# Performance work log

Hardware: AMD Instinct MI355X
Metric: run time of the kernel (lower is better)

## Reference

```python
import jax, jax.numpy as jnp
import numpy as np

HEADS = 8
DIM_HEAD = 64
INNER = HEADS * DIM_HEAD  # 512
EPS = 1e-6


def layer_norm(x, gamma, beta):
    mu = jnp.mean(x, axis=-1, keepdims=True)
    var = jnp.var(x, axis=-1, keepdims=True)
    return (x - mu) * jax.lax.rsqrt(var + EPS) * gamma + beta


def setup_inputs() -> dict:
    key = jax.random.key(0)
    ks = jax.random.split(key, 8)
    b, n = 2, 2048
    s = lambda d: 1.0 / np.sqrt(d)
    return {
        "x": jax.random.normal(ks[0], (b, n, INNER), dtype=jnp.float32),
        # weights stored input-major: y = x @ W
        "w_qkv": jax.random.normal(ks[1], (INNER, 3 * INNER), dtype=jnp.float32) * s(INNER),
        "w_out": jax.random.normal(ks[2], (INNER, INNER), dtype=jnp.float32) * s(INNER),
        "b_out": jax.random.normal(ks[3], (INNER,), dtype=jnp.float32) * 0.01,
        "w_ff1": jax.random.normal(ks[4], (INNER, 4 * INNER), dtype=jnp.float32) * s(INNER),
        "w_ff2": jax.random.normal(ks[5], (4 * INNER, INNER), dtype=jnp.float32) * s(4 * INNER),
        "g1": jnp.ones((INNER,), dtype=jnp.float32),
        "be1": jnp.zeros((INNER,), dtype=jnp.float32),
        "g2": jnp.ones((INNER,), dtype=jnp.float32),
        "be2": jnp.zeros((INNER,), dtype=jnp.float32),
    }


def reference(x, w_qkv, w_out, b_out, w_ff1, w_ff2, g1, be1, g2, be2):
    b, n, _ = x.shape
    scale = DIM_HEAD ** (-0.5)
    qkv = x @ w_qkv  # [b, n, 3*inner]
    qkv = qkv.reshape(b, n, 3, HEADS, DIM_HEAD)
    q = qkv[:, :, 0].transpose(0, 2, 1, 3)  # [b, h, n, d]
    k = qkv[:, :, 1].transpose(0, 2, 1, 3)
    v = qkv[:, :, 2].transpose(0, 2, 1, 3)
    dots = jnp.einsum('bhqd,bhkd->bhqk', q, k) * scale
    attn = jax.nn.softmax(dots, axis=-1)
    out = jnp.einsum('bhqk,bhkd->bhqd', attn, v)
    out = out.transpose(0, 2, 1, 3).reshape(b, n, INNER)
    out = out @ w_out + b_out
    attn_res = layer_norm(x + out, g1, be1)
    # NOTE: no activation between the two FFN linears (faithful to source)
    ff = (attn_res @ w_ff1) @ w_ff2
    return layer_norm(attn_res + ff, g2, be2)
```

## Files before the change

### kernel.cpp

```cpp
#include <hip/hip_runtime.h>
#include <hip/hip_bf16.h>
#include <cstdint>
#include <cstddef>
#include <math.h>

#define HEADS 8
#define DHEAD 64
#define INNER 512
#define BATCH 2
#define SEQ   2048
#define MROWS (BATCH*SEQ)
#define LN_EPS 1e-6f
#define KSPLIT 4
#define KCHUNK (SEQ/KSPLIT)
#define QSCALE 0.18033688011110918f

typedef unsigned short u16;
typedef __attribute__((ext_vector_type(8))) short short8;
typedef __attribute__((ext_vector_type(4))) short short4v;
typedef __attribute__((ext_vector_type(4))) float f32x4;

#define MFMA16(a,b,c) __builtin_amdgcn_mfma_f32_16x16x32_bf16((a),(b),(c),0,0,0)
#if __has_builtin(__builtin_amdgcn_mfma_f32_16x16x16bf16_1k)
#define HAVE_MFMA16K16 1
#define MFMA16K16(a,b,c) __builtin_amdgcn_mfma_f32_16x16x16bf16_1k((a),(b),(c),0,0,0)
#endif

__device__ __forceinline__ float bf2f(u16 u) {
    union { float f; uint32_t i; } x; x.i = ((uint32_t)u) << 16; return x.f;
}
__device__ __forceinline__ u16 f2bf(float f) {
    __hip_bfloat16 h = __float2bfloat16(f);
    return *reinterpret_cast<u16*>(&h);
}
__device__ __forceinline__ void gl_lds16(const void* g, void* l) {
    __builtin_amdgcn_global_load_lds(
        (const __attribute__((address_space(1))) void*)g,
        (__attribute__((address_space(3))) void*)l, 16, 0, 0);
}

__global__ void prep_kernel(const float* __restrict__ x, u16* __restrict__ x_b,
                            const float* __restrict__ w_qkv, u16* __restrict__ w_qkvT,
                            const float* __restrict__ w_out, u16* __restrict__ w_outT,
                            const float* __restrict__ w_ff1, u16* __restrict__ w_ff1T,
                            const float* __restrict__ w_ff2, u16* __restrict__ w_ff2T) {
    __shared__ float T[32][33];
    const int blk = blockIdx.x, tid = threadIdx.x;
    if (blk < 2048) {
        int i = blk * 256 + tid;
        float4 v = reinterpret_cast<const float4*>(x)[i];
        ushort4 o;
        o.x = f2bf(v.x); o.y = f2bf(v.y); o.z = f2bf(v.z); o.w = f2bf(v.w);
        reinterpret_cast<ushort4*>(x_b)[i] = o;
        return;
    }
    const float* B; u16* Bt; int K, N, t;
    if (blk < 2816)      { B = w_qkv; Bt = w_qkvT; K = 512;  N = 1536; t = blk - 2048; }
    else if (blk < 3072) { B = w_out; Bt = w_outT; K = 512;  N = 512;  t = blk - 2816; }
    else if (blk < 4096) { B = w_ff1; Bt = w_ff1T; K = 512;  N = 2048; t = blk - 3072; }
    else                 { B = w_ff2; Bt = w_ff2T; K = 2048; N = 512;  t = blk - 4096; }
    const int nb = N / 32;
    const int n0 = (t % nb) * 32, k0 = (t / nb) * 32;
    const int r = tid >> 3, c = (tid & 7) * 4;
    float4 v = *reinterpret_cast<const float4*>(&B[(size_t)(k0 + r) * N + n0 + c]);
    T[c + 0][r] = v.x; T[c + 1][r] = v.y; T[c + 2][r] = v.z; T[c + 3][r] = v.w;
    __syncthreads();
    ushort4 o;
    o.x = f2bf(T[r][c + 0]); o.y = f2bf(T[r][c + 1]);
    o.z = f2bf(T[r][c + 2]); o.w = f2bf(T[r][c + 3]);
    *reinterpret_cast<ushort4*>(&Bt[(size_t)(n0 + r) * K + k0 + c]) = o;
}

template<int BN, int BK, int EPI>
__global__ __launch_bounds__(256) void gemm_bt(const u16* __restrict__ A,
                                               const u16* __restrict__ Bt,
                                               u16* __restrict__ Cb,
                                               u16* __restrict__ Vt,
                                               int M, int N, int K) {
    constexpr int WN = BN / 2;
    constexpr int NT = WN / 16;
    constexpr int ACH = 128 * BK / 8;
    constexpr int BCH = BN * BK / 8;
    constexpr int CW = BK / 8;
    __shared__ u16 As[128 * BK];
    __shared__ u16 Bs[BN * BK];
    const int tid = threadIdx.x;
    const int wave = tid >> 6, lane = tid & 63;
    const int l15 = lane & 15, quad = lane >> 4;
    const int wm = (wave >> 1) * 64, wn = (wave & 1) * WN;
    const int row0 = blockIdx.y * 128, col0 = blockIdx.x * BN;

    int kbase = 0, kend = K;
    if (EPI == 3) {
        int chunk = K / gridDim.z;
        kbase = blockIdx.z * chunk; kend = kbase + chunk;
    }

    f32x4 acc[4][NT];
    #pragma unroll
    for (int mi = 0; mi < 4; ++mi)
        #pragma unroll
        for (int ni = 0; ni < NT; ++ni)
            #pragma unroll
            for (int e = 0; e < 4; ++e) acc[mi][ni][e] = 0.f;

    for (int k0 = kbase; k0 < kend; k0 += BK) {
        #pragma unroll
        for (int idx0 = 0; idx0 < ACH + BCH; idx0 += 256) {
            int idx = idx0 + tid;
            if (idx < ACH) {
                int r = idx / CW, ic = (idx % CW) * 8;
                gl_lds16(A + (size_t)(row0 + r) * K + k0 + ic, &As[idx * 8]);
            } else {
                int ib = idx - ACH;
                int r = ib / CW, ic = (ib % CW) * 8;
                gl_lds16(Bt + (size_t)(col0 + r) * K + k0 + ic, &Bs[ib * 8]);
            }
        }
        __syncthreads();

        #pragma unroll
        for (int ks2 = 0; ks2 < BK / 32; ++ks2) {
            short8 af[4], bfr[NT];
            #pragma unroll
            for (int mi = 0; mi < 4; ++mi)
                af[mi] = *reinterpret_cast<const short8*>(
                    &As[(wm + mi * 16 + l15) * BK + ks2 * 32 + quad * 8]);
            #pragma unroll
            for (int ni = 0; ni < NT; ++ni)
                bfr[ni] = *reinterpret_cast<const short8*>(
                    &Bs[(wn + ni * 16 + l15) * BK + ks2 * 32 + quad * 8]);
            #pragma unroll
            for (int mi = 0; mi < 4; ++mi)
                #pragma unroll
                for (int ni = 0; ni < NT; ++ni)
                    acc[mi][ni] = MFMA16(af[mi], bfr[ni], acc[mi][ni]);
        }
        __syncthreads();
    }

    #pragma unroll
    for (int mi = 0; mi < 4; ++mi)
        #pragma unroll
        for (int ni = 0; ni < NT; ++ni) {
            const int cc = col0 + wn + ni * 16 + l15;
            const int rr0 = row0 + wm + mi * 16 + quad * 4;
            if (EPI == 0) {
                #pragma unroll
                for (int r = 0; r < 4; ++r)
                    Cb[(size_t)(rr0 + r) * N + cc] = f2bf(acc[mi][ni][r]);
            } else if (EPI == 3) {
                u16* Cz = Cb + (size_t)blockIdx.z * M * N;
                #pragma unroll
                for (int r = 0; r < 4; ++r)
                    Cz[(size_t)(rr0 + r) * N + cc] = f2bf(acc[mi][ni][r]);
            } else {
                if (cc < 1024) {
                    const bool isq = (cc < 512);
                    size_t base = isq ? (size_t)cc
                                      : ((size_t)MROWS * 512 + cc - 512);
                    const float sc = isq ? QSCALE : 1.f;
                    #pragma unroll
                    for (int r = 0; r < 4; ++r)
                        Cb[base + (size_t)(rr0 + r) * 512] = f2bf(acc[mi][ni][r] * sc);
                } else {
                    int hh = (cc - 1024) >> 6, dd = (cc - 1024) & 63;
                    int bb = rr0 >> 11, srow = rr0 & 2047;
                    ushort4 o;
                    o.x = f2bf(acc[mi][ni][0]); o.y = f2bf(acc[mi][ni][1]);
                    o.z = f2bf(acc[mi][ni][2]); o.w = f2bf(acc[mi][ni][3]);
                    *reinterpret_cast<ushort4*>(
                        &Vt[(((size_t)(bb * 8 + hh) * 64 + dd) << 11) + srow]) = o;
                }
            }
        }
}

__global__ __launch_bounds__(256) void attn_kernel(const u16* __restrict__ qk_b,
                                                   const u16* __restrict__ vT_b,
                                                   u16* __restrict__ OpartB,
                                                   float* __restrict__ lpart) {
#ifdef HAVE_MFMA16K16
    __shared__ u16 SM[2 * 64 * 72];
    u16 (*Ks)[72] = (u16(*)[72])SM;
    u16 (*VT)[72] = (u16(*)[72])(SM + 64 * 72);
#else
    __shared__ u16 SM[128 * 64 + 2 * 64 * 72];
    u16 (*Qs)[64] = (u16(*)[64])SM;
    u16 (*Ks)[72] = (u16(*)[72])(SM + 128 * 64);
    u16 (*VT)[72] = (u16(*)[72])(SM + 128 * 64 + 64 * 72);
#endif

    const int tid = threadIdx.x;
    const int wave = tid >> 6, lane = tid & 63;
    const int l15 = lane & 15, quad = lane >> 4;
    const int qt = blockIdx.x, bh = blockIdx.y, ks = blockIdx.z;
    const int b = bh >> 3, h = bh & 7;
    const int w16 = wave * 16;
    const int r0 = tid >> 3, r1 = r0 + 32;
    const int ch = (tid & 7) * 8;

    const u16* qb = qk_b + (size_t)(b * SEQ + qt * 128) * 512 + h * 64;
    const u16* kb = qk_b + (size_t)MROWS * 512
                  + (size_t)(b * SEQ + ks * KCHUNK) * 512 + h * 64;
    const u16* vb = vT_b + (size_t)bh * 64 * 2048 + ks * KCHUNK;

    uint4 kr0 = *reinterpret_cast<const uint4*>(&kb[(size_t)r0 * 512 + ch]);
    uint4 kr1 = *reinterpret_cast<const uint4*>(&kb[(size_t)r1 * 512 + ch]);
    uint4 vr0 = *reinterpret_cast<const uint4*>(&vb[(size_t)r0 * 2048 + ch]);
    uint4 vr1 = *reinterpret_cast<const uint4*>(&vb[(size_t)r1 * 2048 + ch]);

#ifdef HAVE_MFMA16K16
    short8 qf[2][2];
    #pragma unroll
    for (int t = 0; t < 2; ++t)
        #pragma unroll
        for (int ksk = 0; ksk < 2; ++ksk)
            qf[t][ksk] = *reinterpret_cast<const short8*>(
                &qb[(size_t)(t * 64 + w16 + l15) * 512 + ksk * 32 + quad * 8]);

    const short ONEB = (short)0x3F80;
    const short4v ones = {ONEB, ONEB, ONEB, ONEB};

    f32x4 oacc[2][4], lacc[2];
    #pragma unroll
    for (int t = 0; t < 2; ++t) {
        #pragma unroll
        for (int di = 0; di < 4; ++di)
            #pragma unroll
            for (int e = 0; e < 4; ++e) oacc[t][di][e] = 0.f;
        #pragma unroll
        for (int e = 0; e < 4; ++e) lacc[t][e] = 0.f;
    }

    for (int kt = 0; kt < KCHUNK / 64; ++kt) {
        *reinterpret_cast<uint4*>(&Ks[r0][ch]) = kr0;
        *reinterpret_cast<uint4*>(&Ks[r1][ch]) = kr1;
        *reinterpret_cast<uint4*>(&VT[r0][ch]) = vr0;
        *reinterpret_cast<uint4*>(&VT[r1][ch]) = vr1;
        __syncthreads();

        if (kt + 1 < KCHUNK / 64) {
            const u16* kb2 = kb + (size_t)(kt + 1) * 64 * 512;
            const u16* vb2 = vb + (kt + 1) * 64;
            kr0 = *reinterpret_cast<const uint4*>(&kb2[(size_t)r0 * 512 + ch]);
            kr1 = *reinterpret_cast<const uint4*>(&kb2[(size_t)r1 * 512 + ch]);
            vr0 = *reinterpret_cast<const uint4*>(&vb2[(size_t)r0 * 2048 + ch]);
            vr1 = *reinterpret_cast<const uint4*>(&vb2[(size_t)r1 * 2048 + ch]);
        }

        short8 kf[4], kf2[4];
        #pragma unroll
        for (int ni = 0; ni < 4; ++ni) {
            kf[ni]  = *reinterpret_cast<const short8*>(&Ks[ni * 16 + l15][quad * 8]);
            kf2[ni] = *reinterpret_cast<const short8*>(&Ks[ni * 16 + l15][32 + quad * 8]);
        }

        #pragma unroll
        for (int t = 0; t < 2; ++t) {
            f32x4 sacc[4];
            #pragma unroll
            for (int ni = 0; ni < 4; ++ni)
                #pragma unroll
                for (int e = 0; e < 4; ++e) sacc[ni][e] = 0.f;
            #pragma unroll
            for (int ni = 0; ni < 4; ++ni)
                sacc[ni] = MFMA16(kf[ni], qf[t][0], sacc[ni]);
            #pragma unroll
            for (int ni = 0; ni < 4; ++ni)
                sacc[ni] = MFMA16(kf2[ni], qf[t][1], sacc[ni]);

            #pragma unroll
            for (int ni = 0; ni < 4; ++ni) {
                float p0 = exp2f(sacc[ni][0]);
                float p1 = exp2f(sacc[ni][1]);
                float p2 = exp2f(sacc[ni][2]);
                float p3 = exp2f(sacc[ni][3]);
                union { short4v v; uint32_t u[2]; } P;
                P.u[0] = __builtin_amdgcn_perm(__float_as_uint(p1),
                                               __float_as_uint(p0), 0x07060302u);
                P.u[1] = __builtin_amdgcn_perm(__float_as_uint(p3),
                                               __float_as_uint(p2), 0x07060302u);
                lacc[t] = MFMA16K16(ones, P.v, lacc[t]);
                #pragma unroll
                for (int di = 0; di < 4; ++di) {
                    short4v vf = *reinterpret_cast<const short4v*>(
                        &VT[di * 16 + l15][ni * 16 + quad * 4]);
                    oacc[t][di] = MFMA16K16(vf, P.v, oacc[t][di]);
                }
            }
        }
        __syncthreads();
    }

    const size_t pbase = ((size_t)(ks * 16 + bh) * SEQ + qt * 128);
    if (lane < 16) {
        lpart[pbase + w16 + lane]      = lacc[0][0];
        lpart[pbase + 64 + w16 + lane] = lacc[1][0];
    }

    float* OTf = (float*)SM;
    const int ql = tid >> 2, dseg = (tid & 3) * 16;
    #pragma unroll
    for (int t = 0; t < 2; ++t) {
        __syncthreads();
        #pragma unroll
        for (int di = 0; di < 4; ++di)
            #pragma unroll
            for (int r = 0; r < 4; ++r)
                OTf[(di * 16 + quad * 4 + r) * 68 + w16 + l15] = oacc[t][di][r];
        __syncthreads();
        u16 ov[16];
        #pragma unroll
        for (int i = 0; i < 16; ++i) ov[i] = f2bf(OTf[(dseg + i) * 68 + ql]);
        u16* op = &OpartB[(pbase + t * 64 + ql) * 64 + dseg];
        *reinterpret_cast<uint4*>(op)     = *reinterpret_cast<const uint4*>(ov);
        *reinterpret_cast<uint4*>(op + 8) = *reinterpret_cast<const uint4*>(ov + 8);
    }
#else
    {
        #pragma unroll
        for (int j = 0; j < 4; ++j) {
            int idx = tid + j * 256;
            int r = idx >> 3, c = (idx & 7) * 8;
            *reinterpret_cast<uint4*>(&Qs[r][c]) =
                *reinterpret_cast<const uint4*>(&qb[(size_t)r * 512 + c]);
        }
    }
    __syncthreads();

    short8 qf[2][2];
    #pragma unroll
    for (int t = 0; t < 2; ++t) {
        qf[t][0] = *reinterpret_cast<const short8*>(&Qs[t * 64 + w16 + l15][quad * 8]);
        qf[t][1] = *reinterpret_cast<const short8*>(&Qs[t * 64 + w16 + l15][32 + quad * 8]);
    }

    f32x4 oacc[2][4];
    float lsum[2][4];
    #pragma unroll
    for (int t = 0; t < 2; ++t)
        #pragma unroll
        for (int di = 0; di < 4; ++di) {
            #pragma unroll
            for (int e = 0; e < 4; ++e) oacc[t][di][e] = 0.f;
            lsum[t][di] = 0.f;
        }

    for (int kt = 0; kt < KCHUNK / 64; ++kt) {
        *reinterpret_cast<uint4*>(&Ks[r0][ch]) = kr0;
        *reinterpret_cast<uint4*>(&Ks[r1][ch]) = kr1;
        *reinterpret_cast<uint4*>(&VT[r0][ch]) = vr0;
        *reinterpret_cast<uint4*>(&VT[r1][ch]) = vr1;
        __syncthreads();

        if (kt + 1 < KCHUNK / 64) {
            const u16* kb2 = kb + (size_t)(kt + 1) * 64 * 512;
            const u16* vb2 = vb + (kt + 1) * 64;
            kr0 = *reinterpret_cast<const uint4*>(&kb2[(size_t)r0 * 512 + ch]);
            kr1 = *reinterpret_cast<const uint4*>(&kb2[(size_t)r1 * 512 + ch]);
            vr0 = *reinterpret_cast<const uint4*>(&vb2[(size_t)r0 * 2048 + ch]);
            vr1 = *reinterpret_cast<const uint4*>(&vb2[(size_t)r1 * 2048 + ch]);
        }

        #pragma unroll
        for (int t = 0; t < 2; ++t) {
            f32x4 sacc[4];
            #pragma unroll
            for (int ni = 0; ni < 4; ++ni)
                #pragma unroll
                for (int e = 0; e < 4; ++e) sacc[ni][e] = 0.f;
            #pragma unroll
            for (int ksk = 0; ksk < 2; ++ksk) {
                short8 kf[4];
                #pragma unroll
                for (int ni = 0; ni < 4; ++ni)
                    kf[ni] = *reinterpret_cast<const short8*>(
                        &Ks[ni * 16 + l15][ksk * 32 + quad * 8]);
                #pragma unroll
                for (int ni = 0; ni < 4; ++ni)
                    sacc[ni] = MFMA16(qf[t][ksk], kf[ni], sacc[ni]);
            }
            #pragma unroll
            for (int ni = 0; ni < 4; ++ni)
                #pragma unroll
                for (int r = 0; r < 4; ++r) {
                    float p = exp2f(sacc[ni][r]);
                    lsum[t][r] += p;
                    Qs[t * 64 + w16 + quad * 4 + r][ni * 16 + l15] = f2bf(p);
                }
            #pragma unroll
            for (int ksk = 0; ksk < 2; ++ksk) {
                short8 pf = *reinterpret_cast<const short8*>(
                    &Qs[t * 64 + w16 + l15][ksk * 32 + quad * 8]);
                #pragma unroll
                for (int di = 0; di < 4; ++di) {
                    short8 vf = *reinterpret_cast<const short8*>(
                        &VT[di * 16 + l15][ksk * 32 + quad * 8]);
                    oacc[t][di] = MFMA16(pf, vf, oacc[t][di]);
                }
            }
        }
        __syncthreads();
    }

    const size_t pbase = ((size_t)(ks * 16 + bh) * SEQ + qt * 128);
    #pragma unroll
    for (int t = 0; t < 2; ++t) {
        #pragma unroll
        for (int r = 0; r < 4; ++r) {
            float v = lsum[t][r];
            v += __shfl_xor(v, 1); v += __shfl_xor(v, 2);
            v += __shfl_xor(v, 4); v += __shfl_xor(v, 8);
            lsum[t][r] = v;
        }
        #pragma unroll
        for (int di = 0; di < 4; ++di)
            #pragma unroll
            for (int r = 0; r < 4; ++r)
                OpartB[(pbase + t * 64 + w16 + quad * 4 + r) * 64 + di * 16 + l15]
                    = f2bf(oacc[t][di][r]);
        if (l15 == 0)
            #pragma unroll
            for (int r = 0; r < 4; ++r)
                lpart[pbase + t * 64 + w16 + quad * 4 + r] = lsum[t][r];
    }
#endif
}

__global__ void attn_combine_kernel(const u16* __restrict__ OpartB,
                                    const float* __restrict__ lpart,
                                    u16* __restrict__ attn_b) {
    int i = blockIdx.x * 256 + threadIdx.x;
    int e = i * 4;
    int row = e >> 9;
    int c = e & 511;
    int h = c >> 6, d = c & 63;
    int b = row >> 11, srow = row & 2047;
    int bh = b * 8 + h;

    float ax = 0.f, ay = 0.f, az = 0.f, aw = 0.f, l = 0.f;
    #pragma unroll
    for (int ks = 0; ks < KSPLIT; ++ks) {
        size_t pk = (size_t)(ks * 16 + bh) * SEQ + srow;
        ushort4 o = *reinterpret_cast<const ushort4*>(&OpartB[pk * 64 + d]);
        ax += bf2f(o.x); ay += bf2f(o.y); az += bf2f(o.z); aw += bf2f(o.w);
        l += lpart[pk];
    }
    float li = 1.f / l;
    ushort4 o;
    o.x = f2bf(ax * li); o.y = f2bf(ay * li);
    o.z = f2bf(az * li); o.w = f2bf(aw * li);
    *reinterpret_cast<ushort4*>(&attn_b[(size_t)row * INNER + c]) = o;
}

template<bool A16, int NS>
__global__ __launch_bounds__(256) void ln_kernel(const void* __restrict__ a_,
                                                 const u16* __restrict__ s_,
                                                 size_t sstride,
                                                 const float* __restrict__ bias,
                                                 const float* __restrict__ g,
                                                 const float* __restrict__ be,
                                                 float* __restrict__ out32,
                                                 u16* __restrict__ out16) {
    const int tid = threadIdx.x, wave = tid >> 6, lane = tid & 63;
    const int row = blockIdx.x * 4 + wave;
    const size_t off = (size_t)row * INNER;

    float v[8];
    #pragma unroll
    for (int j = 0; j < 2; ++j) {
        const int c = j * 256 + lane * 4;
        if (A16) {
            ushort4 u = *reinterpret_cast<const ushort4*>((const u16*)a_ + off + c);
            v[j*4+0] = bf2f(u.x); v[j*4+1] = bf2f(u.y);
            v[j*4+2] = bf2f(u.z); v[j*4+3] = bf2f(u.w);
        } else {
            float4 u = *reinterpret_cast<const float4*>((const float*)a_ + off + c);
            v[j*4+0] = u.x; v[j*4+1] = u.y; v[j*4+2] = u.z; v[j*4+3] = u.w;
        }
        #pragma unroll
        for (int s = 0; s < NS; ++s) {
            ushort4 u = *reinterpret_cast<const ushort4*>(
                s_ + (size_t)s * sstride + off + c);
            v[j*4+0] += bf2f(u.x); v[j*4+1] += bf2f(u.y);
            v[j*4+2] += bf2f(u.z); v[j*4+3] += bf2f(u.w);
        }
        if (bias) {
            float4 u = *reinterpret_cast<const float4*>(bias + c);
            v[j*4+0] += u.x; v[j*4+1] += u.y; v[j*4+2] += u.z; v[j*4+3] += u.w;
        }
    }

    float s = 0.f;
    #pragma unroll
    for (int i = 0; i < 8; ++i) s += v[i];
    #pragma unroll
    for (int m = 1; m < 64; m <<= 1) s += __shfl_xor(s, m);
    const float mu = s * (1.f / INNER);

    float q = 0.f;
    #pragma unroll
    for (int i = 0; i < 8; ++i) { v[i] -= mu; q += v[i] * v[i]; }
    #pragma unroll
    for (int m = 1; m < 64; m <<= 1) q += __shfl_xor(q, m);
    const float rstd = rsqrtf(q * (1.f / INNER) + LN_EPS);

    #pragma unroll
    for (int j = 0; j < 2; ++j) {
        const int c = j * 256 + lane * 4;
        float4 gv = *reinterpret_cast<const float4*>(g + c);
        float4 bv = *reinterpret_cast<const float4*>(be + c);
        float y0 = v[j*4+0] * rstd * gv.x + bv.x;
        float y1 = v[j*4+1] * rstd * gv.y + bv.y;
        float y2 = v[j*4+2] * rstd * gv.z + bv.z;
        float y3 = v[j*4+3] * rstd * gv.w + bv.w;
        if (out32) {
            float4 o = {y0, y1, y2, y3};
            *reinterpret_cast<float4*>(out32 + off + c) = o;
        }
        if (out16) {
            ushort4 o;
            o.x = f2bf(y0); o.y = f2bf(y1); o.z = f2bf(y2); o.w = f2bf(y3);
            *reinterpret_cast<ushort4*>(out16 + off + c) = o;
        }
    }
}

extern "C" void kernel_launch(void* const* d_in, const int* in_sizes, int n_in,
                              void* d_out, int out_size, void* d_ws, size_t ws_size,
                              hipStream_t stream) {
    const float* x     = (const float*)d_in[0];
    const float* w_qkv = (const float*)d_in[1];
    const float* w_out = (const float*)d_in[2];
    const float* b_out = (const float*)d_in[3];
    const float* w_ff1 = (const float*)d_in[4];
    const float* w_ff2 = (const float*)d_in[5];
    const float* g1    = (const float*)d_in[6];
    const float* be1   = (const float*)d_in[7];
    const float* g2    = (const float*)d_in[8];
    const float* be2   = (const float*)d_in[9];
    float* out = (float*)d_out;

    char* W = (char*)d_ws;
    u16*   w_outT     = (u16*)  (W + 0);
    u16*   w_ff1T     = (u16*)  (W + 524288);
    u16*   w_ff2T     = (u16*)  (W + 2621440);
    u16*   qk_b       = (u16*)  (W + 4718592);
    u16*   projp      = (u16*)  (W + 4718592);
    u16*   vT_b       = (u16*)  (W + 13107200);
    u16*   attn_res_b = (u16*)  (W + 13107200);
    u16*   x_b        = (u16*)  (W + 17301504);
    u16*   w_qkvT     = (u16*)  (W + 21495808);
    u16*   OpartB     = (u16*)  (W + 23068672);
    float* lpart      = (float*)(W + 39845888);
    u16*   attn_b     = (u16*)  (W + 40370176);
    u16*   ff1_b      = (u16*)  (W + 17301504);
    u16*   ff2p       = (u16*)  (W + 40370176);

    prep_kernel<<<5120, 256, 0, stream>>>(x, x_b, w_qkv, w_qkvT, w_out, w_outT,
                                          w_ff1, w_ff1T, w_ff2, w_ff2T);

    gemm_bt<64, 64, 2><<<dim3(1536 / 64, MROWS / 128), 256, 0, stream>>>(
        x_b, w_qkvT, qk_b, vT_b, MROWS, 1536, INNER);

    attn_kernel<<<dim3(SEQ / 128, BATCH * HEADS, KSPLIT), 256, 0, stream>>>(
        qk_b, vT_b, OpartB, lpart);

    attn_combine_kernel<<<(MROWS * INNER / 4) / 256, 256, 0, stream>>>(
        OpartB, lpart, attn_b);

    gemm_bt<64, 64, 3><<<dim3(INNER / 64, MROWS / 128, 2), 256, 0, stream>>>(
        attn_b, w_outT, projp, nullptr, MROWS, INNER, INNER);

    ln_kernel<true, 2><<<MROWS / 4, 256, 0, stream>>>(
        x_b, projp, (size_t)MROWS * INNER, b_out, g1, be1, nullptr, attn_res_b);

    gemm_bt<128, 64, 0><<<dim3(2048 / 128, MROWS / 128), 256, 0, stream>>>(
        attn_res_b, w_ff1T, ff1_b, nullptr, MROWS, 2048, INNER);

    gemm_bt<64, 64, 3><<<dim3(INNER / 64, MROWS / 128, 4), 256, 0, stream>>>(
        ff1_b, w_ff2T, ff2p, nullptr, MROWS, INNER, 2048);

    ln_kernel<true, 4><<<MROWS / 4, 256, 0, stream>>>(
        attn_res_b, ff2p, (size_t)MROWS * INNER, nullptr, g2, be2, out, nullptr);
}
```

Measured before the change: 204.8 us.

## Shrink attention query tile to 64 and double key split to 8

The attention kernel now processes 64 query rows per block instead of 128, and the key sequence is split into 8 chunks instead of 4. The grid grows from 1024 to 4096 blocks, with less work and fewer live registers per block, to raise occupancy and parallelism. In exchange each K/V tile is loaded and reused for half as many queries, and the combine step must read and merge twice as many partial outputs. Workspace buffers are re-laid out so the larger partial-output and normalizer arrays fit.

```diff
diff --git a/kernel.cpp b/kernel.cpp
--- a/kernel.cpp
+++ b/kernel.cpp
@@ -11,7 +11,7 @@
 #define SEQ   2048
 #define MROWS (BATCH*SEQ)
 #define LN_EPS 1e-6f
-#define KSPLIT 4
+#define KSPLIT 8
 #define KCHUNK (SEQ/KSPLIT)
 #define QSCALE 0.18033688011110918f
 
@@ -185,10 +185,10 @@
     u16 (*Ks)[72] = (u16(*)[72])SM;
     u16 (*VT)[72] = (u16(*)[72])(SM + 64 * 72);
 #else
-    __shared__ u16 SM[128 * 64 + 2 * 64 * 72];
+    __shared__ u16 SM[64 * 64 + 2 * 64 * 72];
     u16 (*Qs)[64] = (u16(*)[64])SM;
-    u16 (*Ks)[72] = (u16(*)[72])(SM + 128 * 64);
-    u16 (*VT)[72] = (u16(*)[72])(SM + 128 * 64 + 64 * 72);
+    u16 (*Ks)[72] = (u16(*)[72])(SM + 64 * 64);
+    u16 (*VT)[72] = (u16(*)[72])(SM + 64 * 64 + 64 * 72);
 #endif
 
     const int tid = threadIdx.x;
@@ -199,8 +199,9 @@
     const int w16 = wave * 16;
     const int r0 = tid >> 3, r1 = r0 + 32;
     const int ch = (tid & 7) * 8;
-
-    const u16* qb = qk_b + (size_t)(b * SEQ + qt * 128) * 512 + h * 64;
+    constexpr int NT = KCHUNK / 64;
+
+    const u16* qb = qk_b + (size_t)(b * SEQ + qt * 64) * 512 + h * 64;
     const u16* kb = qk_b + (size_t)MROWS * 512
                   + (size_t)(b * SEQ + ks * KCHUNK) * 512 + h * 64;
     const u16* vb = vT_b + (size_t)bh * 64 * 2048 + ks * KCHUNK;
@@ -211,36 +212,29 @@
     uint4 vr1 = *reinterpret_cast<const uint4*>(&vb[(size_t)r1 * 2048 + ch]);
 
 #ifdef HAVE_MFMA16K16
-    short8 qf[2][2];
-    #pragma unroll
-    for (int t = 0; t < 2; ++t)
-        #pragma unroll
-        for (int ksk = 0; ksk < 2; ++ksk)
-            qf[t][ksk] = *reinterpret_cast<const short8*>(
-                &qb[(size_t)(t * 64 + w16 + l15) * 512 + ksk * 32 + quad * 8]);
+    short8 qf[2];
+    qf[0] = *reinterpret_cast<const short8*>(&qb[(size_t)(w16 + l15) * 512 + quad * 8]);
+    qf[1] = *reinterpret_cast<const short8*>(&qb[(size_t)(w16 + l15) * 512 + 32 + quad * 8]);
 
     const short ONEB = (short)0x3F80;
     const short4v ones = {ONEB, ONEB, ONEB, ONEB};
 
-    f32x4 oacc[2][4], lacc[2];
-    #pragma unroll
-    for (int t = 0; t < 2; ++t) {
-        #pragma unroll
-        for (int di = 0; di < 4; ++di)
-            #pragma unroll
-            for (int e = 0; e < 4; ++e) oacc[t][di][e] = 0.f;
-        #pragma unroll
-        for (int e = 0; e < 4; ++e) lacc[t][e] = 0.f;
-    }
-
-    for (int kt = 0; kt < KCHUNK / 64; ++kt) {
+    f32x4 oacc[4], lacc;
+    #pragma unroll
+    for (int di = 0; di < 4; ++di)
+        #pragma unroll
+        for (int e = 0; e < 4; ++e) oacc[di][e] = 0.f;
+    #pragma unroll
+    for (int e = 0; e < 4; ++e) lacc[e] = 0.f;
+
+    for (int kt = 0; kt < NT; ++kt) {
         *reinterpret_cast<uint4*>(&Ks[r0][ch]) = kr0;
         *reinterpret_cast<uint4*>(&Ks[r1][ch]) = kr1;
         *reinterpret_cast<uint4*>(&VT[r0][ch]) = vr0;
         *reinterpret_cast<uint4*>(&VT[r1][ch]) = vr1;
         __syncthreads();
 
-        if (kt + 1 < KCHUNK / 64) {
+        if (kt + 1 < NT) {
             const u16* kb2 = kb + (size_t)(kt + 1) * 64 * 512;
             const u16* vb2 = vb + (kt + 1) * 64;
             kr0 = *reinterpret_cast<const uint4*>(&kb2[(size_t)r0 * 512 + ch]);
@@ -249,78 +243,70 @@
             vr1 = *reinterpret_cast<const uint4*>(&vb2[(size_t)r1 * 2048 + ch]);
         }
 
-        short8 kf[4], kf2[4];
+        f32x4 sacc[4];
+        #pragma unroll
+        for (int ni = 0; ni < 4; ++ni)
+            #pragma unroll
+            for (int e = 0; e < 4; ++e) sacc[ni][e] = 0.f;
+        {
+            short8 kf[4], kf2[4];
+            #pragma unroll
+            for (int ni = 0; ni < 4; ++ni) {
+                kf[ni]  = *reinterpret_cast<const short8*>(&Ks[ni * 16 + l15][quad * 8]);
+                kf2[ni] = *reinterpret_cast<const short8*>(&Ks[ni * 16 + l15][32 + quad * 8]);
+            }
+            #pragma unroll
+            for (int ni = 0; ni < 4; ++ni)
+                sacc[ni] = MFMA16(kf[ni], qf[0], sacc[ni]);
+            #pragma unroll
+            for (int ni = 0; ni < 4; ++ni)
+                sacc[ni] = MFMA16(kf2[ni], qf[1], sacc[ni]);
+        }
+
         #pragma unroll
         for (int ni = 0; ni < 4; ++ni) {
-            kf[ni]  = *reinterpret_cast<const short8*>(&Ks[ni * 16 + l15][quad * 8]);
-            kf2[ni] = *reinterpret_cast<const short8*>(&Ks[ni * 16 + l15][32 + quad * 8]);
-        }
-
-        #pragma unroll
-        for (int t = 0; t < 2; ++t) {
-            f32x4 sacc[4];
-            #pragma unroll
-            for (int ni = 0; ni < 4; ++ni)
-                #pragma unroll
-                for (int e = 0; e < 4; ++e) sacc[ni][e] = 0.f;
-            #pragma unroll
-            for (int ni = 0; ni < 4; ++ni)
-                sacc[ni] = MFMA16(kf[ni], qf[t][0], sacc[ni]);
-            #pragma unroll
-            for (int ni = 0; ni < 4; ++ni)
-                sacc[ni] = MFMA16(kf2[ni], qf[t][1], sacc[ni]);
-
-            #pragma unroll
-            for (int ni = 0; ni < 4; ++ni) {
-                float p0 = exp2f(sacc[ni][0]);
-                float p1 = exp2f(sacc[ni][1]);
-                float p2 = exp2f(sacc[ni][2]);
-                float p3 = exp2f(sacc[ni][3]);
-                union { short4v v; uint32_t u[2]; } P;
-                P.u[0] = __builtin_amdgcn_perm(__float_as_uint(p1),
-                                               __float_as_uint(p0), 0x07060302u);
-                P.u[1] = __builtin_amdgcn_perm(__float_as_uint(p3),
-                                               __float_as_uint(p2), 0x07060302u);
-                lacc[t] = MFMA16K16(ones, P.v, lacc[t]);
-                #pragma unroll
-                for (int di = 0; di < 4; ++di) {
-                    short4v vf = *reinterpret_cast<const short4v*>(
-                        &VT[di * 16 + l15][ni * 16 + quad * 4]);
-                    oacc[t][di] = MFMA16K16(vf, P.v, oacc[t][di]);
-                }
+            float p0 = exp2f(sacc[ni][0]);
+            float p1 = exp2f(sacc[ni][1]);
+            float p2 = exp2f(sacc[ni][2]);
+            float p3 = exp2f(sacc[ni][3]);
+            union { short4v v; uint32_t u[2]; } P;
+            P.u[0] = __builtin_amdgcn_perm(__float_as_uint(p1),
+                                           __float_as_uint(p0), 0x07060302u);
+            P.u[1] = __builtin_amdgcn_perm(__float_as_uint(p3),
+                                           __float_as_uint(p2), 0x07060302u);
+            lacc = MFMA16K16(ones, P.v, lacc);
+            #pragma unroll
+            for (int di = 0; di < 4; ++di) {
+                short4v vf = *reinterpret_cast<const short4v*>(
+                    &VT[di * 16 + l15][ni * 16 + quad * 4]);
+                oacc[di] = MFMA16K16(vf, P.v, oacc[di]);
             }
         }
         __syncthreads();
     }
 
-    const size_t pbase = ((size_t)(ks * 16 + bh) * SEQ + qt * 128);
-    if (lane < 16) {
-        lpart[pbase + w16 + lane]      = lacc[0][0];
-        lpart[pbase + 64 + w16 + lane] = lacc[1][0];
-    }
+    const size_t pbase = ((size_t)(ks * 16 + bh) * SEQ + qt * 64);
+    if (lane < 16) lpart[pbase + w16 + lane] = lacc[0];
 
     float* OTf = (float*)SM;
+    #pragma unroll
+    for (int di = 0; di < 4; ++di)
+        #pragma unroll
+        for (int r = 0; r < 4; ++r)
+            OTf[(di * 16 + quad * 4 + r) * 68 + w16 + l15] = oacc[di][r];
+    __syncthreads();
+
     const int ql = tid >> 2, dseg = (tid & 3) * 16;
-    #pragma unroll
-    for (int t = 0; t < 2; ++t) {
-        __syncthreads();
-        #pragma unroll
-        for (int di = 0; di < 4; ++di)
-            #pragma unroll
-            for (int r = 0; r < 4; ++r)
-                OTf[(di * 16 + quad * 4 + r) * 68 + w16 + l15] = oacc[t][di][r];
-        __syncthreads();
-        u16 ov[16];
-        #pragma unroll
-        for (int i = 0; i < 16; ++i) ov[i] = f2bf(OTf[(dseg + i) * 68 + ql]);
-        u16* op = &OpartB[(pbase + t * 64 + ql) * 64 + dseg];
-        *reinterpret_cast<uint4*>(op)     = *reinterpret_cast<const uint4*>(ov);
-        *reinterpret_cast<uint4*>(op + 8) = *reinterpret_cast<const uint4*>(ov + 8);
-    }
+    u16 ov[16];
+    #pragma unroll
+    for (int i = 0; i < 16; ++i) ov[i] = f2bf(OTf[(dseg + i) * 68 + ql]);
+    u16* op = &OpartB[(pbase + ql) * 64 + dseg];
+    *reinterpret_cast<uint4*>(op)     = *reinterpret_cast<const uint4*>(ov);
+    *reinterpret_cast<uint4*>(op + 8) = *reinterpret_cast<const uint4*>(ov + 8);
 #else
     {
         #pragma unroll
-        for (int j = 0; j < 4; ++j) {
+        for (int j = 0; j < 2; ++j) {
             int idx = tid + j * 256;
             int r = idx >> 3, c = (idx & 7) * 8;
             *reinterpret_cast<uint4*>(&Qs[r][c]) =
@@ -329,32 +315,27 @@
     }
     __syncthreads();
 
-    short8 qf[2][2];
-    #pragma unroll
-    for (int t = 0; t < 2; ++t) {
-        qf[t][0] = *reinterpret_cast<const short8*>(&Qs[t * 64 + w16 + l15][quad * 8]);
-        qf[t][1] = *reinterpret_cast<const short8*>(&Qs[t * 64 + w16 + l15][32 + quad * 8]);
-    }
-
-    f32x4 oacc[2][4];
-    float lsum[2][4];
-    #pragma unroll
-    for (int t = 0; t < 2; ++t)
-        #pragma unroll
-        for (int di = 0; di < 4; ++di) {
-            #pragma unroll
-            for (int e = 0; e < 4; ++e) oacc[t][di][e] = 0.f;
-            lsum[t][di] = 0.f;
-        }
-
-    for (int kt = 0; kt < KCHUNK / 64; ++kt) {
+    short8 qf[2];
+    qf[0] = *reinterpret_cast<const short8*>(&Qs[w16 + l15][quad * 8]);
+    qf[1] = *reinterpret_cast<const short8*>(&Qs[w16 + l15][32 + quad * 8]);
+
+    f32x4 oacc[4];
+    float lsum[4];
+    #pragma unroll
+    for (int di = 0; di < 4; ++di) {
+        #pragma unroll
+        for (int e = 0; e < 4; ++e) oacc[di][e] = 0.f;
+        lsum[di] = 0.f;
+    }
+
+    for (int kt = 0; kt < NT; ++kt) {
         *reinterpret_cast<uint4*>(&Ks[r0][ch]) = kr0;
         *reinterpret_cast<uint4*>(&Ks[r1][ch]) = kr1;
         *reinterpret_cast<uint4*>(&VT[r0][ch]) = vr0;
         *reinterpret_cast<uint4*>(&VT[r1][ch]) = vr1;
         __syncthreads();
 
-        if (kt + 1 < KCHUNK / 64) {
+        if (kt + 1 < NT) {
             const u16* kb2 = kb + (size_t)(kt + 1) * 64 * 512;
             const u16* vb2 = vb + (kt + 1) * 64;
             kr0 = *reinterpret_cast<const uint4*>(&kb2[(size_t)r0 * 512 + ch]);
@@ -363,68 +344,62 @@
             vr1 = *reinterpret_cast<const uint4*>(&vb2[(size_t)r1 * 2048 + ch]);
         }
 
-        #pragma unroll
-        for (int t = 0; t < 2; ++t) {
-            f32x4 sacc[4];
+        f32x4 sacc[4];
+        #pragma unroll
+        for (int ni = 0; ni < 4; ++ni)
+            #pragma unroll
+            for (int e = 0; e < 4; ++e) sacc[ni][e] = 0.f;
+        #pragma unroll
+        for (int ksk = 0; ksk < 2; ++ksk) {
+            short8 kf[4];
             #pragma unroll
             for (int ni = 0; ni < 4; ++ni)
-                #pragma unroll
-                for (int e = 0; e < 4; ++e) sacc[ni][e] = 0.f;
-            #pragma unroll
-            for (int ksk = 0; ksk < 2; ++ksk) {
-                short8 kf[4];
-                #pragma unroll
-                for (int ni = 0; ni < 4; ++ni)
-                    kf[ni] = *reinterpret_cast<const short8*>(
-                        &Ks[ni * 16 + l15][ksk * 32 + quad * 8]);
-                #pragma unroll
-                for (int ni = 0; ni < 4; ++ni)
-                    sacc[ni] = MFMA16(qf[t][ksk], kf[ni], sacc[ni]);
+                kf[ni] = *reinterpret_cast<const short8*>(
+                    &Ks[ni * 16 + l15][ksk * 32 + quad * 8]);
+            #pragma unroll
+            for (int ni = 0; ni < 4; ++ni)
+                sacc[ni] = MFMA16(qf[ksk], kf[ni], sacc[ni]);
+        }
+        #pragma unroll
+        for (int ni = 0; ni < 4; ++ni)
+            #pragma unroll
+            for (int r = 0; r < 4; ++r) {
+                float p = exp2f(sacc[ni][r]);
+                lsum[r] += p;
+                Qs[w16 + quad * 4 + r][ni * 16 + l15] = f2bf(p);
             }
-            #pragma unroll
-            for (int ni = 0; ni < 4; ++ni)
-                #pragma unroll
-                for (int r = 0; r < 4; ++r) {
-                    float p = exp2f(sacc[ni][r]);
-                    lsum[t][r] += p;
-                    Qs[t * 64 + w16 + quad * 4 + r][ni * 16 + l15] = f2bf(p);
-                }
-            #pragma unroll
-            for (int ksk = 0; ksk < 2; ++ksk) {
-                short8 pf = *reinterpret_cast<const short8*>(
-                    &Qs[t * 64 + w16 + l15][ksk * 32 + quad * 8]);
-                #pragma unroll
-                for (int di = 0; di < 4; ++di) {
-                    short8 vf = *reinterpret_cast<const short8*>(
-                        &VT[di * 16 + l15][ksk * 32 + quad * 8]);
-                    oacc[t][di] = MFMA16(pf, vf, oacc[t][di]);
-                }
+        #pragma unroll
+        for (int ksk = 0; ksk < 2; ++ksk) {
+            short8 pf = *reinterpret_cast<const short8*>(
+                &Qs[w16 + l15][ksk * 32 + quad * 8]);
+            #pragma unroll
+            for (int di = 0; di < 4; ++di) {
+                short8 vf = *reinterpret_cast<const short8*>(
+                    &VT[di * 16 + l15][ksk * 32 + quad * 8]);
+                oacc[di] = MFMA16(pf, vf, oacc[di]);
             }
         }
         __syncthreads();
     }
 
-    const size_t pbase = ((size_t)(ks * 16 + bh) * SEQ + qt * 128);
-    #pragma unroll
-    for (int t = 0; t < 2; ++t) {
-        #pragma unroll
-        for (int r = 0; r < 4; ++r) {
-            float v = lsum[t][r];
-            v += __shfl_xor(v, 1); v += __shfl_xor(v, 2);
-            v += __shfl_xor(v, 4); v += __shfl_xor(v, 8);
-            lsum[t][r] = v;
-        }
-        #pragma unroll
-        for (int di = 0; di < 4; ++di)
-            #pragma unroll
-            for (int r = 0; r < 4; ++r)
-                OpartB[(pbase + t * 64 + w16 + quad * 4 + r) * 64 + di * 16 + l15]
-                    = f2bf(oacc[t][di][r]);
-        if (l15 == 0)
-            #pragma unroll
-            for (int r = 0; r < 4; ++r)
-                lpart[pbase + t * 64 + w16 + quad * 4 + r] = lsum[t][r];
-    }
+    const size_t pbase = ((size_t)(ks * 16 + bh) * SEQ + qt * 64);
+    #pragma unroll
+    for (int r = 0; r < 4; ++r) {
+        float v = lsum[r];
+        v += __shfl_xor(v, 1); v += __shfl_xor(v, 2);
+        v += __shfl_xor(v, 4); v += __shfl_xor(v, 8);
+        lsum[r] = v;
+    }
+    #pragma unroll
+    for (int di = 0; di < 4; ++di)
+        #pragma unroll
+        for (int r = 0; r < 4; ++r)
+            OpartB[(pbase + w16 + quad * 4 + r) * 64 + di * 16 + l15]
+                = f2bf(oacc[di][r]);
+    if (l15 == 0)
+        #pragma unroll
+        for (int r = 0; r < 4; ++r)
+            lpart[pbase + w16 + quad * 4 + r] = lsum[r];
 #endif
 }
 
@@ -549,14 +524,14 @@
     u16*   qk_b       = (u16*)  (W + 4718592);
     u16*   projp      = (u16*)  (W + 4718592);
     u16*   vT_b       = (u16*)  (W + 13107200);
+    u16*   attn_b     = (u16*)  (W + 13107200);
     u16*   attn_res_b = (u16*)  (W + 13107200);
     u16*   x_b        = (u16*)  (W + 17301504);
     u16*   w_qkvT     = (u16*)  (W + 21495808);
+    float* lpart      = (float*)(W + 21495808);
     u16*   OpartB     = (u16*)  (W + 23068672);
-    float* lpart      = (float*)(W + 39845888);
-    u16*   attn_b     = (u16*)  (W + 40370176);
     u16*   ff1_b      = (u16*)  (W + 17301504);
-    u16*   ff2p       = (u16*)  (W + 40370176);
+    u16*   ff2p       = (u16*)  (W + 34078720);
 
     prep_kernel<<<5120, 256, 0, stream>>>(x, x_b, w_qkv, w_qkvT, w_out, w_outT,
                                           w_ff1, w_ff1T, w_ff2, w_ff2T);
@@ -564,7 +539,7 @@
     gemm_bt<64, 64, 2><<<dim3(1536 / 64, MROWS / 128), 256, 0, stream>>>(
         x_b, w_qkvT, qk_b, vT_b, MROWS, 1536, INNER);
 
-    attn_kernel<<<dim3(SEQ / 128, BATCH * HEADS, KSPLIT), 256, 0, stream>>>(
+    attn_kernel<<<dim3(SEQ / 64, BATCH * HEADS, KSPLIT), 256, 0, stream>>>(
         qk_b, vT_b, OpartB, lpart);
 
     attn_combine_kernel<<<(MROWS * INNER / 4) / 256, 256, 0, stream>>>(
```

After: 209.6 us. 1.02x slower.
